# Optimization experiments

Measured on AMD Instinct MI355X. Metric: run time of the kernel, lower is better.

## Reference

```python
import jax, jax.numpy as jnp
import numpy as np

N_SRC = 50000
N_DST = 50000
D = 64
E = 800000


def setup_inputs() -> dict:
    key = jax.random.key(0)
    k1, k2, k3, k4, k5 = jax.random.split(key, 5)
    return {
        "h_src": jax.random.normal(k1, (N_SRC, D), dtype=jnp.float32),
        "h_dst": jax.random.normal(k2, (N_DST, D), dtype=jnp.float32),
        "src_idx": jax.random.randint(k3, (E,), 0, N_SRC, dtype=jnp.int64)
        if jax.config.read("jax_enable_x64")
        else jax.random.randint(k3, (E,), 0, N_SRC, dtype=jnp.int32),
        "dst_idx": jax.random.randint(k4, (E,), 0, N_DST, dtype=jnp.int32),
        "W_src": jax.random.normal(k5, (D, D), dtype=jnp.float32) * (2.0 / np.sqrt(2 * D)),  # xavier_normal w/ relu gain
        "b_src": jnp.zeros((D,), dtype=jnp.float32),
    }


def reference(h_src, h_dst, src_idx, dst_idx, W_src, b_src):
    # --- edge attention logits: u_mul_v (elementwise), shape [E, D] ---
    e = h_src[src_idx] * h_dst[dst_idx]
    # --- edge_softmax: softmax over incoming edges of each dst node, per feature dim ---
    emax = jax.ops.segment_max(e, dst_idx, num_segments=N_DST)  # [N_dst, D]
    emax = jnp.where(jnp.isfinite(emax), emax, 0.0)  # empty segments -> -inf; neutralize
    ex = jnp.exp(e - emax[dst_idx])  # [E, D]
    denom = jax.ops.segment_sum(ex, dst_idx, num_segments=N_DST)  # [N_dst, D]
    alpha = ex / denom[dst_idx]  # [E, D]
    # --- transformed src features: relu(W x + b), viewed as [N_src, H=1, D] ---
    feat_src = jax.nn.relu(h_src @ W_src.T + b_src)  # [N_src, D]
    # --- u_mul_e + sum aggregation (H=1 broadcast) ---
    m = feat_src[src_idx] * alpha  # [E, D]
    rst = jax.ops.segment_sum(m, dst_idx, num_segments=N_DST)  # [N_dst, D]
    return rst[:, None, :]  # [N_dst, num_heads=1, out_feats] (dropout in eval mode)
```

## Files before the change

### kernel.cpp

```cpp
#include <hip/hip_runtime.h>
#include <math.h>
#include <stdint.h>

#define D 64
#define WSZ 32
#define WSHIFT 5
#define QCAP 1024
#define EPT 16
#define NWMAX 2048

typedef __attribute__((ext_vector_type(8))) short bf16x8;
typedef __attribute__((ext_vector_type(4))) float f32x4;

__device__ inline ushort bf16_rne_u(float v) {
    uint32_t u = __float_as_uint(v);
    return (ushort)((u + 0x7FFFu + ((u >> 16) & 1u)) >> 16);
}

__global__ __launch_bounds__(256) void prep_kernel(const float* __restrict__ h,
                                                   const float* __restrict__ W,
                                                   const float* __restrict__ b,
                                                   const int* __restrict__ src_idx,
                                                   const int* __restrict__ dst_idx,
                                                   uint32_t* __restrict__ packed,
                                                   int* __restrict__ qcnt,
                                                   uint32_t* __restrict__ queue,
                                                   int Nsrc, int Ndst, int E, int packBlocks) {
    __shared__ ushort hT[64 * 64];
    __shared__ ushort wT[64 * 64];
    __shared__ float bs[64];
    __shared__ int wcount[NWMAX];
    __shared__ int wbase[NWMAX];

    if ((int)blockIdx.x < packBlocks) {
        const int t = threadIdx.x;
        const int R0 = blockIdx.x * 64;

        if (t < 64) bs[t] = b[t];
#pragma unroll
        for (int k = 0; k < 4; ++k) {
            int f4 = k * 256 + t;
            int row = f4 >> 4;
            int c4 = (f4 & 15) * 4;
            int grow = min(R0 + row, Nsrc - 1);
            float4 v = reinterpret_cast<const float4*>(h)[(size_t)grow * 16 + (f4 & 15)];
            hT[row * 64 + c4 + 0] = bf16_rne_u(v.x);
            hT[row * 64 + c4 + 1] = bf16_rne_u(v.y);
            hT[row * 64 + c4 + 2] = bf16_rne_u(v.z);
            hT[row * 64 + c4 + 3] = bf16_rne_u(v.w);
            float4 w = reinterpret_cast<const float4*>(W)[f4];
            wT[row * 64 + c4 + 0] = bf16_rne_u(w.x);
            wT[row * 64 + c4 + 1] = bf16_rne_u(w.y);
            wT[row * 64 + c4 + 2] = bf16_rne_u(w.z);
            wT[row * 64 + c4 + 3] = bf16_rne_u(w.w);
        }
        __syncthreads();

        const int wave = t >> 6;
        const int lane = t & 63;
        const int m = lane & 15;
        const int quad = lane >> 4;

        bf16x8 afrag[2];
#pragma unroll
        for (int ks = 0; ks < 2; ++ks)
            afrag[ks] = *reinterpret_cast<const bf16x8*>(&hT[(wave * 16 + m) * 64 + ks * 32 + quad * 8]);

#pragma unroll
        for (int nt = 0; nt < 4; ++nt) {
            const int c0 = nt * 16;
            f32x4 acc = {0.f, 0.f, 0.f, 0.f};
#pragma unroll
            for (int ks = 0; ks < 2; ++ks) {
                bf16x8 bfrag = *reinterpret_cast<const bf16x8*>(&wT[(c0 + m) * 64 + ks * 32 + quad * 8]);
                acc = __builtin_amdgcn_mfma_f32_16x16x32_bf16(afrag[ks], bfrag, acc, 0, 0, 0);
            }
            const int col = c0 + m;
            const float bias = bs[col];
#pragma unroll
            for (int reg = 0; reg < 4; ++reg) {
                const int tr = wave * 16 + quad * 4 + reg;
                const int row = R0 + tr;
                if (row < Nsrc) {
                    float f = fmaxf(acc[reg] + bias, 0.f);
                    uint32_t val = (uint32_t)hT[tr * 64 + col] | ((uint32_t)bf16_rne_u(f) << 16);
                    __builtin_nontemporal_store(val, &packed[(size_t)row * D + col]);
                }
            }
        }
    } else {
        const int bid = (int)blockIdx.x - packBlocks;
        const int t = threadIdx.x;
        for (int k = t; k < NWMAX; k += 256) wcount[k] = 0;
        __syncthreads();

        const int i = bid * 256 + t;
        const int e0 = i * EPT;
        const bool full = (e0 + EPT <= E);

        int4 d0, d1, d2, d3, s0, s1, s2, s3;
        if (full) {
            const int4* dp = reinterpret_cast<const int4*>(dst_idx) + i * 4;
            const int4* sp = reinterpret_cast<const int4*>(src_idx) + i * 4;
            d0 = dp[0]; d1 = dp[1]; d2 = dp[2]; d3 = dp[3];
            s0 = sp[0]; s1 = sp[1]; s2 = sp[2]; s3 = sp[3];
            atomicAdd(&wcount[d0.x >> WSHIFT], 1); atomicAdd(&wcount[d0.y >> WSHIFT], 1);
            atomicAdd(&wcount[d0.z >> WSHIFT], 1); atomicAdd(&wcount[d0.w >> WSHIFT], 1);
            atomicAdd(&wcount[d1.x >> WSHIFT], 1); atomicAdd(&wcount[d1.y >> WSHIFT], 1);
            atomicAdd(&wcount[d1.z >> WSHIFT], 1); atomicAdd(&wcount[d1.w >> WSHIFT], 1);
            atomicAdd(&wcount[d2.x >> WSHIFT], 1); atomicAdd(&wcount[d2.y >> WSHIFT], 1);
            atomicAdd(&wcount[d2.z >> WSHIFT], 1); atomicAdd(&wcount[d2.w >> WSHIFT], 1);
            atomicAdd(&wcount[d3.x >> WSHIFT], 1); atomicAdd(&wcount[d3.y >> WSHIFT], 1);
            atomicAdd(&wcount[d3.z >> WSHIFT], 1); atomicAdd(&wcount[d3.w >> WSHIFT], 1);
        } else {
            for (int e = e0; e < E; ++e) atomicAdd(&wcount[dst_idx[e] >> WSHIFT], 1);
        }
        __syncthreads();

        for (int k = t; k < NWMAX; k += 256) {
            int c = wcount[k];
            wbase[k] = (c > 0) ? atomicAdd(&qcnt[k], c) : 0;
        }
        __syncthreads();

#define EMIT(dv, sv)                                                            \
        {                                                                       \
            int w_ = (dv) >> WSHIFT;                                            \
            int pos_ = atomicAdd(&wbase[w_], 1);                                \
            if (pos_ < QCAP)                                                    \
                queue[(size_t)w_ * QCAP + pos_] =                               \
                    (uint32_t)(sv) | ((uint32_t)((dv) & (WSZ - 1)) << 16);      \
        }
        if (full) {
            EMIT(d0.x, s0.x) EMIT(d0.y, s0.y) EMIT(d0.z, s0.z) EMIT(d0.w, s0.w)
            EMIT(d1.x, s1.x) EMIT(d1.y, s1.y) EMIT(d1.z, s1.z) EMIT(d1.w, s1.w)
            EMIT(d2.x, s2.x) EMIT(d2.y, s2.y) EMIT(d2.z, s2.z) EMIT(d2.w, s2.w)
            EMIT(d3.x, s3.x) EMIT(d3.y, s3.y) EMIT(d3.z, s3.z) EMIT(d3.w, s3.w)
        } else {
            for (int e = e0; e < E; ++e) { EMIT(dst_idx[e], src_idx[e]) }
        }
#undef EMIT
    }
}

__device__ inline void stepd(uint32_t u, float y, float& l, float& a) {
    float x = __uint_as_float(u << 16);
    float f = __uint_as_float(u & 0xFFFF0000u);
    float pe = __expf(x * y);
    l += pe;
    a += pe * f;
}

__device__ inline void step4(uint4 u, const float4& y, float4& l, float4& a) {
    stepd(u.x, y.x, l.x, a.x);
    stepd(u.y, y.y, l.y, a.y);
    stepd(u.z, y.z, l.z, a.z);
    stepd(u.w, y.w, l.w, a.w);
}

__global__ __launch_bounds__(256) void sortmain_kernel(const uint32_t* __restrict__ queue,
                                                       const int* __restrict__ qcnt,
                                                       const uint32_t* __restrict__ packed,
                                                       const float* __restrict__ h_dst,
                                                       float* __restrict__ out, int Ndst) {
    __shared__ uint32_t ent[QCAP];
    __shared__ ushort srt[QCAP];
    __shared__ int hist[WSZ], sc[WSZ], cur[WSZ];
    const int w = blockIdx.x;
    const int t = threadIdx.x;
    const int n = min(qcnt[w], QCAP);

    for (int k = t; k < n; k += 256) ent[k] = queue[(size_t)w * QCAP + k];
    if (t < WSZ) hist[t] = 0;
    __syncthreads();
    for (int k = t; k < n; k += 256) atomicAdd(&hist[(ent[k] >> 16) & (WSZ - 1)], 1);
    __syncthreads();
    if (t < WSZ) sc[t] = hist[t];
    __syncthreads();
    for (int off = 1; off < WSZ; off <<= 1) {
        int v = (t >= off && t < WSZ) ? sc[t - off] : 0;
        __syncthreads();
        if (t < WSZ) sc[t] += v;
        __syncthreads();
    }
    if (t < WSZ) cur[t] = sc[t] - hist[t];
    __syncthreads();
    for (int k = t; k < n; k += 256) {
        uint32_t e = ent[k];
        int dl = (e >> 16) & (WSZ - 1);
        int pos = atomicAdd(&cur[dl], 1);
        srt[pos] = (ushort)(e & 0xFFFFu);
    }
    __syncthreads();

    const int g = t >> 4;
    const int q = t & 15;
#pragma unroll
    for (int rep = 0; rep < WSZ / 16; ++rep) {
        const int dl = rep * 16 + g;
        const int j = w * WSZ + dl;
        if (j >= Ndst) continue;

        const float4 y = reinterpret_cast<const float4*>(h_dst + (size_t)j * D)[q];
        const int cnt = hist[dl];
        const int base = sc[dl] - cnt;

        float4 l0 = make_float4(0.f, 0.f, 0.f, 0.f), a0 = l0;
        float4 l1 = l0, a1 = l0, l2 = l0, a2 = l0, l3 = l0, a3 = l0;

        int p = 0;
        for (; p + 3 < cnt; p += 4) {
            uint32_t s0 = srt[base + p], s1 = srt[base + p + 1];
            uint32_t s2 = srt[base + p + 2], s3 = srt[base + p + 3];
            uint4 u0 = reinterpret_cast<const uint4*>(packed + (size_t)s0 * D)[q];
            uint4 u1 = reinterpret_cast<const uint4*>(packed + (size_t)s1 * D)[q];
            uint4 u2 = reinterpret_cast<const uint4*>(packed + (size_t)s2 * D)[q];
            uint4 u3 = reinterpret_cast<const uint4*>(packed + (size_t)s3 * D)[q];
            step4(u0, y, l0, a0);
            step4(u1, y, l1, a1);
            step4(u2, y, l2, a2);
            step4(u3, y, l3, a3);
        }
        for (; p < cnt; ++p) {
            uint32_t s0 = srt[base + p];
            uint4 u0 = reinterpret_cast<const uint4*>(packed + (size_t)s0 * D)[q];
            step4(u0, y, l0, a0);
        }

        l0.x += l1.x + l2.x + l3.x; a0.x += a1.x + a2.x + a3.x;
        l0.y += l1.y + l2.y + l3.y; a0.y += a1.y + a2.y + a3.y;
        l0.z += l1.z + l2.z + l3.z; a0.z += a1.z + a2.z + a3.z;
        l0.w += l1.w + l2.w + l3.w; a0.w += a1.w + a2.w + a3.w;

        float4 o;
        o.x = (l0.x > 0.f) ? a0.x / l0.x : 0.f;
        o.y = (l0.y > 0.f) ? a0.y / l0.y : 0.f;
        o.z = (l0.z > 0.f) ? a0.z / l0.z : 0.f;
        o.w = (l0.w > 0.f) ? a0.w / l0.w : 0.f;
        reinterpret_cast<float4*>(out + (size_t)j * D)[q] = o;
    }
}

extern "C" void kernel_launch(void* const* d_in, const int* in_sizes, int n_in,
                              void* d_out, int out_size, void* d_ws, size_t ws_size,
                              hipStream_t stream) {
    const float* h_src = (const float*)d_in[0];
    const float* h_dst = (const float*)d_in[1];
    const int* src_idx = (const int*)d_in[2];
    const int* dst_idx = (const int*)d_in[3];
    const float* W_src = (const float*)d_in[4];
    const float* b_src = (const float*)d_in[5];
    float* out = (float*)d_out;

    const int Nsrc = in_sizes[0] / D;
    const int Ndst = in_sizes[1] / D;
    const int E = in_sizes[2];
    const int NW = (Ndst + WSZ - 1) >> WSHIFT;

    const int packBlocks = (Nsrc + 63) / 64;
    const int binBlocks = (E + 256 * EPT - 1) / (256 * EPT);

    uint32_t* packed   = (uint32_t*)d_ws;
    int*      qcnt     = (int*)(packed + (size_t)Nsrc * D);
    uint32_t* queue    = (uint32_t*)(qcnt + NWMAX);

    hipMemsetAsync(qcnt, 0, sizeof(int) * NWMAX, stream);

    prep_kernel<<<packBlocks + binBlocks, 256, 0, stream>>>(
        h_src, W_src, b_src, src_idx, dst_idx, packed, qcnt, queue,
        Nsrc, Ndst, E, packBlocks);
    sortmain_kernel<<<NW, 256, 0, stream>>>(queue, qcnt, packed, h_dst, out, Ndst);
}
```

Baseline: 127.1 us.

## Fuse prep and sort/aggregate kernels into one cooperative persistent kernel

Merges the pack/bin kernel and the per-window sort+aggregate kernel into a single persistent cooperative kernel. Blocks loop over tasks, then meet at a grid-wide sync instead of a kernel boundary, with shared memory unioned across phases. This removes one kernel launch and its drain and fill, at the cost of a grid barrier and a grid capped at the occupancy limit. It also drops the nontemporal store on packed so the data can stay in cache for the gather phase.

```diff
diff --git a/kernel.cpp b/kernel.cpp
--- a/kernel.cpp
+++ b/kernel.cpp
@@ -1,6 +1,9 @@
 #include <hip/hip_runtime.h>
+#include <hip/hip_cooperative_groups.h>
 #include <math.h>
 #include <stdint.h>
+
+namespace cg = cooperative_groups;
 
 #define D 64
 #define WSZ 32
@@ -17,132 +20,6 @@
     return (ushort)((u + 0x7FFFu + ((u >> 16) & 1u)) >> 16);
 }
 
-__global__ __launch_bounds__(256) void prep_kernel(const float* __restrict__ h,
-                                                   const float* __restrict__ W,
-                                                   const float* __restrict__ b,
-                                                   const int* __restrict__ src_idx,
-                                                   const int* __restrict__ dst_idx,
-                                                   uint32_t* __restrict__ packed,
-                                                   int* __restrict__ qcnt,
-                                                   uint32_t* __restrict__ queue,
-                                                   int Nsrc, int Ndst, int E, int packBlocks) {
-    __shared__ ushort hT[64 * 64];
-    __shared__ ushort wT[64 * 64];
-    __shared__ float bs[64];
-    __shared__ int wcount[NWMAX];
-    __shared__ int wbase[NWMAX];
-
-    if ((int)blockIdx.x < packBlocks) {
-        const int t = threadIdx.x;
-        const int R0 = blockIdx.x * 64;
-
-        if (t < 64) bs[t] = b[t];
-#pragma unroll
-        for (int k = 0; k < 4; ++k) {
-            int f4 = k * 256 + t;
-            int row = f4 >> 4;
-            int c4 = (f4 & 15) * 4;
-            int grow = min(R0 + row, Nsrc - 1);
-            float4 v = reinterpret_cast<const float4*>(h)[(size_t)grow * 16 + (f4 & 15)];
-            hT[row * 64 + c4 + 0] = bf16_rne_u(v.x);
-            hT[row * 64 + c4 + 1] = bf16_rne_u(v.y);
-            hT[row * 64 + c4 + 2] = bf16_rne_u(v.z);
-            hT[row * 64 + c4 + 3] = bf16_rne_u(v.w);
-            float4 w = reinterpret_cast<const float4*>(W)[f4];
-            wT[row * 64 + c4 + 0] = bf16_rne_u(w.x);
-            wT[row * 64 + c4 + 1] = bf16_rne_u(w.y);
-            wT[row * 64 + c4 + 2] = bf16_rne_u(w.z);
-            wT[row * 64 + c4 + 3] = bf16_rne_u(w.w);
-        }
-        __syncthreads();
-
-        const int wave = t >> 6;
-        const int lane = t & 63;
-        const int m = lane & 15;
-        const int quad = lane >> 4;
-
-        bf16x8 afrag[2];
-#pragma unroll
-        for (int ks = 0; ks < 2; ++ks)
-            afrag[ks] = *reinterpret_cast<const bf16x8*>(&hT[(wave * 16 + m) * 64 + ks * 32 + quad * 8]);
-
-#pragma unroll
-        for (int nt = 0; nt < 4; ++nt) {
-            const int c0 = nt * 16;
-            f32x4 acc = {0.f, 0.f, 0.f, 0.f};
-#pragma unroll
-            for (int ks = 0; ks < 2; ++ks) {
-                bf16x8 bfrag = *reinterpret_cast<const bf16x8*>(&wT[(c0 + m) * 64 + ks * 32 + quad * 8]);
-                acc = __builtin_amdgcn_mfma_f32_16x16x32_bf16(afrag[ks], bfrag, acc, 0, 0, 0);
-            }
-            const int col = c0 + m;
-            const float bias = bs[col];
-#pragma unroll
-            for (int reg = 0; reg < 4; ++reg) {
-                const int tr = wave * 16 + quad * 4 + reg;
-                const int row = R0 + tr;
-                if (row < Nsrc) {
-                    float f = fmaxf(acc[reg] + bias, 0.f);
-                    uint32_t val = (uint32_t)hT[tr * 64 + col] | ((uint32_t)bf16_rne_u(f) << 16);
-                    __builtin_nontemporal_store(val, &packed[(size_t)row * D + col]);
-                }
-            }
-        }
-    } else {
-        const int bid = (int)blockIdx.x - packBlocks;
-        const int t = threadIdx.x;
-        for (int k = t; k < NWMAX; k += 256) wcount[k] = 0;
-        __syncthreads();
-
-        const int i = bid * 256 + t;
-        const int e0 = i * EPT;
-        const bool full = (e0 + EPT <= E);
-
-        int4 d0, d1, d2, d3, s0, s1, s2, s3;
-        if (full) {
-            const int4* dp = reinterpret_cast<const int4*>(dst_idx) + i * 4;
-            const int4* sp = reinterpret_cast<const int4*>(src_idx) + i * 4;
-            d0 = dp[0]; d1 = dp[1]; d2 = dp[2]; d3 = dp[3];
-            s0 = sp[0]; s1 = sp[1]; s2 = sp[2]; s3 = sp[3];
-            atomicAdd(&wcount[d0.x >> WSHIFT], 1); atomicAdd(&wcount[d0.y >> WSHIFT], 1);
-            atomicAdd(&wcount[d0.z >> WSHIFT], 1); atomicAdd(&wcount[d0.w >> WSHIFT], 1);
-            atomicAdd(&wcount[d1.x >> WSHIFT], 1); atomicAdd(&wcount[d1.y >> WSHIFT], 1);
-            atomicAdd(&wcount[d1.z >> WSHIFT], 1); atomicAdd(&wcount[d1.w >> WSHIFT], 1);
-            atomicAdd(&wcount[d2.x >> WSHIFT], 1); atomicAdd(&wcount[d2.y >> WSHIFT], 1);
-            atomicAdd(&wcount[d2.z >> WSHIFT], 1); atomicAdd(&wcount[d2.w >> WSHIFT], 1);
-            atomicAdd(&wcount[d3.x >> WSHIFT], 1); atomicAdd(&wcount[d3.y >> WSHIFT], 1);
-            atomicAdd(&wcount[d3.z >> WSHIFT], 1); atomicAdd(&wcount[d3.w >> WSHIFT], 1);
-        } else {
-            for (int e = e0; e < E; ++e) atomicAdd(&wcount[dst_idx[e] >> WSHIFT], 1);
-        }
-        __syncthreads();
-
-        for (int k = t; k < NWMAX; k += 256) {
-            int c = wcount[k];
-            wbase[k] = (c > 0) ? atomicAdd(&qcnt[k], c) : 0;
-        }
-        __syncthreads();
-
-#define EMIT(dv, sv)                                                            \
-        {                                                                       \
-            int w_ = (dv) >> WSHIFT;                                            \
-            int pos_ = atomicAdd(&wbase[w_], 1);                                \
-            if (pos_ < QCAP)                                                    \
-                queue[(size_t)w_ * QCAP + pos_] =                               \
-                    (uint32_t)(sv) | ((uint32_t)((dv) & (WSZ - 1)) << 16);      \
-        }
-        if (full) {
-            EMIT(d0.x, s0.x) EMIT(d0.y, s0.y) EMIT(d0.z, s0.z) EMIT(d0.w, s0.w)
-            EMIT(d1.x, s1.x) EMIT(d1.y, s1.y) EMIT(d1.z, s1.z) EMIT(d1.w, s1.w)
-            EMIT(d2.x, s2.x) EMIT(d2.y, s2.y) EMIT(d2.z, s2.z) EMIT(d2.w, s2.w)
-            EMIT(d3.x, s3.x) EMIT(d3.y, s3.y) EMIT(d3.z, s3.z) EMIT(d3.w, s3.w)
-        } else {
-            for (int e = e0; e < E; ++e) { EMIT(dst_idx[e], src_idx[e]) }
-        }
-#undef EMIT
-    }
-}
-
 __device__ inline void stepd(uint32_t u, float y, float& l, float& a) {
     float x = __uint_as_float(u << 16);
     float f = __uint_as_float(u & 0xFFFF0000u);
@@ -158,86 +35,214 @@
     stepd(u.w, y.w, l.w, a.w);
 }
 
-__global__ __launch_bounds__(256) void sortmain_kernel(const uint32_t* __restrict__ queue,
-                                                       const int* __restrict__ qcnt,
-                                                       const uint32_t* __restrict__ packed,
-                                                       const float* __restrict__ h_dst,
-                                                       float* __restrict__ out, int Ndst) {
-    __shared__ uint32_t ent[QCAP];
-    __shared__ ushort srt[QCAP];
-    __shared__ int hist[WSZ], sc[WSZ], cur[WSZ];
-    const int w = blockIdx.x;
+__global__ __launch_bounds__(256, 4) void fused_kernel(
+        const float* __restrict__ h, const float* __restrict__ W,
+        const float* __restrict__ b,
+        const int* __restrict__ src_idx, const int* __restrict__ dst_idx,
+        const float* __restrict__ h_dst,
+        uint32_t* __restrict__ packed, int* __restrict__ qcnt,
+        uint32_t* __restrict__ queue, float* __restrict__ out,
+        int Nsrc, int Ndst, int E, int packBlocks, int binBlocks, int NW) {
+    __shared__ union {
+        struct { ushort hT[64 * 64]; ushort wT[64 * 64]; float bs[64]; } pk;
+        struct { int wcount[NWMAX]; int wbase[NWMAX]; } bn;
+        struct { uint32_t ent[QCAP]; ushort srt[QCAP];
+                 int hist[WSZ]; int sc[WSZ]; int cur[WSZ]; } sm;
+    } u;
+
     const int t = threadIdx.x;
-    const int n = min(qcnt[w], QCAP);
-
-    for (int k = t; k < n; k += 256) ent[k] = queue[(size_t)w * QCAP + k];
-    if (t < WSZ) hist[t] = 0;
-    __syncthreads();
-    for (int k = t; k < n; k += 256) atomicAdd(&hist[(ent[k] >> 16) & (WSZ - 1)], 1);
-    __syncthreads();
-    if (t < WSZ) sc[t] = hist[t];
-    __syncthreads();
-    for (int off = 1; off < WSZ; off <<= 1) {
-        int v = (t >= off && t < WSZ) ? sc[t - off] : 0;
-        __syncthreads();
-        if (t < WSZ) sc[t] += v;
-        __syncthreads();
+    const int tasks = packBlocks + binBlocks;
+
+    for (int task = blockIdx.x; task < tasks; task += gridDim.x) {
+        __syncthreads();
+        if (task < packBlocks) {
+            const int R0 = task * 64;
+            if (t < 64) u.pk.bs[t] = b[t];
+#pragma unroll
+            for (int k = 0; k < 4; ++k) {
+                int f4 = k * 256 + t;
+                int row = f4 >> 4;
+                int c4 = (f4 & 15) * 4;
+                int grow = min(R0 + row, Nsrc - 1);
+                float4 v = reinterpret_cast<const float4*>(h)[(size_t)grow * 16 + (f4 & 15)];
+                u.pk.hT[row * 64 + c4 + 0] = bf16_rne_u(v.x);
+                u.pk.hT[row * 64 + c4 + 1] = bf16_rne_u(v.y);
+                u.pk.hT[row * 64 + c4 + 2] = bf16_rne_u(v.z);
+                u.pk.hT[row * 64 + c4 + 3] = bf16_rne_u(v.w);
+                float4 w = reinterpret_cast<const float4*>(W)[f4];
+                u.pk.wT[row * 64 + c4 + 0] = bf16_rne_u(w.x);
+                u.pk.wT[row * 64 + c4 + 1] = bf16_rne_u(w.y);
+                u.pk.wT[row * 64 + c4 + 2] = bf16_rne_u(w.z);
+                u.pk.wT[row * 64 + c4 + 3] = bf16_rne_u(w.w);
+            }
+            __syncthreads();
+
+            const int wave = t >> 6;
+            const int lane = t & 63;
+            const int m = lane & 15;
+            const int quad = lane >> 4;
+
+            bf16x8 afrag[2];
+#pragma unroll
+            for (int ks = 0; ks < 2; ++ks)
+                afrag[ks] = *reinterpret_cast<const bf16x8*>(
+                    &u.pk.hT[(wave * 16 + m) * 64 + ks * 32 + quad * 8]);
+
+#pragma unroll
+            for (int nt = 0; nt < 4; ++nt) {
+                const int c0 = nt * 16;
+                f32x4 acc = {0.f, 0.f, 0.f, 0.f};
+#pragma unroll
+                for (int ks = 0; ks < 2; ++ks) {
+                    bf16x8 bfrag = *reinterpret_cast<const bf16x8*>(
+                        &u.pk.wT[(c0 + m) * 64 + ks * 32 + quad * 8]);
+                    acc = __builtin_amdgcn_mfma_f32_16x16x32_bf16(afrag[ks], bfrag, acc, 0, 0, 0);
+                }
+                const int col = c0 + m;
+                const float bias = u.pk.bs[col];
+#pragma unroll
+                for (int reg = 0; reg < 4; ++reg) {
+                    const int tr = wave * 16 + quad * 4 + reg;
+                    const int row = R0 + tr;
+                    if (row < Nsrc) {
+                        float f = fmaxf(acc[reg] + bias, 0.f);
+                        uint32_t val = (uint32_t)u.pk.hT[tr * 64 + col] |
+                                       ((uint32_t)bf16_rne_u(f) << 16);
+                        packed[(size_t)row * D + col] = val;
+                    }
+                }
+            }
+        } else {
+            const int bid = task - packBlocks;
+            for (int k = t; k < NWMAX; k += 256) u.bn.wcount[k] = 0;
+            __syncthreads();
+
+            const int i = bid * 256 + t;
+            const int e0 = i * EPT;
+            const bool full = (e0 + EPT <= E);
+
+            int4 d0, d1, d2, d3, s0, s1, s2, s3;
+            if (full) {
+                const int4* dp = reinterpret_cast<const int4*>(dst_idx) + i * 4;
+                const int4* sp = reinterpret_cast<const int4*>(src_idx) + i * 4;
+                d0 = dp[0]; d1 = dp[1]; d2 = dp[2]; d3 = dp[3];
+                s0 = sp[0]; s1 = sp[1]; s2 = sp[2]; s3 = sp[3];
+                atomicAdd(&u.bn.wcount[d0.x >> WSHIFT], 1); atomicAdd(&u.bn.wcount[d0.y >> WSHIFT], 1);
+                atomicAdd(&u.bn.wcount[d0.z >> WSHIFT], 1); atomicAdd(&u.bn.wcount[d0.w >> WSHIFT], 1);
+                atomicAdd(&u.bn.wcount[d1.x >> WSHIFT], 1); atomicAdd(&u.bn.wcount[d1.y >> WSHIFT], 1);
+                atomicAdd(&u.bn.wcount[d1.z >> WSHIFT], 1); atomicAdd(&u.bn.wcount[d1.w >> WSHIFT], 1);
+                atomicAdd(&u.bn.wcount[d2.x >> WSHIFT], 1); atomicAdd(&u.bn.wcount[d2.y >> WSHIFT], 1);
+                atomicAdd(&u.bn.wcount[d2.z >> WSHIFT], 1); atomicAdd(&u.bn.wcount[d2.w >> WSHIFT], 1);
+                atomicAdd(&u.bn.wcount[d3.x >> WSHIFT], 1); atomicAdd(&u.bn.wcount[d3.y >> WSHIFT], 1);
+                atomicAdd(&u.bn.wcount[d3.z >> WSHIFT], 1); atomicAdd(&u.bn.wcount[d3.w >> WSHIFT], 1);
+            } else {
+                for (int e = e0; e < E; ++e) atomicAdd(&u.bn.wcount[dst_idx[e] >> WSHIFT], 1);
+            }
+            __syncthreads();
+
+            for (int k = t; k < NWMAX; k += 256) {
+                int c = u.bn.wcount[k];
+                u.bn.wbase[k] = (c > 0) ? atomicAdd(&qcnt[k], c) : 0;
+            }
+            __syncthreads();
+
+#define EMIT(dv, sv)                                                            \
+            {                                                                   \
+                int w_ = (dv) >> WSHIFT;                                        \
+                int pos_ = atomicAdd(&u.bn.wbase[w_], 1);                       \
+                if (pos_ < QCAP)                                                \
+                    queue[(size_t)w_ * QCAP + pos_] =                           \
+                        (uint32_t)(sv) | ((uint32_t)((dv) & (WSZ - 1)) << 16);  \
+            }
+            if (full) {
+                EMIT(d0.x, s0.x) EMIT(d0.y, s0.y) EMIT(d0.z, s0.z) EMIT(d0.w, s0.w)
+                EMIT(d1.x, s1.x) EMIT(d1.y, s1.y) EMIT(d1.z, s1.z) EMIT(d1.w, s1.w)
+                EMIT(d2.x, s2.x) EMIT(d2.y, s2.y) EMIT(d2.z, s2.z) EMIT(d2.w, s2.w)
+                EMIT(d3.x, s3.x) EMIT(d3.y, s3.y) EMIT(d3.z, s3.z) EMIT(d3.w, s3.w)
+            } else {
+                for (int e = e0; e < E; ++e) { EMIT(dst_idx[e], src_idx[e]) }
+            }
+#undef EMIT
+        }
     }
-    if (t < WSZ) cur[t] = sc[t] - hist[t];
-    __syncthreads();
-    for (int k = t; k < n; k += 256) {
-        uint32_t e = ent[k];
-        int dl = (e >> 16) & (WSZ - 1);
-        int pos = atomicAdd(&cur[dl], 1);
-        srt[pos] = (ushort)(e & 0xFFFFu);
-    }
-    __syncthreads();
+
+    __threadfence();
+    cg::this_grid().sync();
 
     const int g = t >> 4;
     const int q = t & 15;
-#pragma unroll
-    for (int rep = 0; rep < WSZ / 16; ++rep) {
-        const int dl = rep * 16 + g;
-        const int j = w * WSZ + dl;
-        if (j >= Ndst) continue;
-
-        const float4 y = reinterpret_cast<const float4*>(h_dst + (size_t)j * D)[q];
-        const int cnt = hist[dl];
-        const int base = sc[dl] - cnt;
-
-        float4 l0 = make_float4(0.f, 0.f, 0.f, 0.f), a0 = l0;
-        float4 l1 = l0, a1 = l0, l2 = l0, a2 = l0, l3 = l0, a3 = l0;
-
-        int p = 0;
-        for (; p + 3 < cnt; p += 4) {
-            uint32_t s0 = srt[base + p], s1 = srt[base + p + 1];
-            uint32_t s2 = srt[base + p + 2], s3 = srt[base + p + 3];
-            uint4 u0 = reinterpret_cast<const uint4*>(packed + (size_t)s0 * D)[q];
-            uint4 u1 = reinterpret_cast<const uint4*>(packed + (size_t)s1 * D)[q];
-            uint4 u2 = reinterpret_cast<const uint4*>(packed + (size_t)s2 * D)[q];
-            uint4 u3 = reinterpret_cast<const uint4*>(packed + (size_t)s3 * D)[q];
-            step4(u0, y, l0, a0);
-            step4(u1, y, l1, a1);
-            step4(u2, y, l2, a2);
-            step4(u3, y, l3, a3);
-        }
-        for (; p < cnt; ++p) {
-            uint32_t s0 = srt[base + p];
-            uint4 u0 = reinterpret_cast<const uint4*>(packed + (size_t)s0 * D)[q];
-            step4(u0, y, l0, a0);
-        }
-
-        l0.x += l1.x + l2.x + l3.x; a0.x += a1.x + a2.x + a3.x;
-        l0.y += l1.y + l2.y + l3.y; a0.y += a1.y + a2.y + a3.y;
-        l0.z += l1.z + l2.z + l3.z; a0.z += a1.z + a2.z + a3.z;
-        l0.w += l1.w + l2.w + l3.w; a0.w += a1.w + a2.w + a3.w;
-
-        float4 o;
-        o.x = (l0.x > 0.f) ? a0.x / l0.x : 0.f;
-        o.y = (l0.y > 0.f) ? a0.y / l0.y : 0.f;
-        o.z = (l0.z > 0.f) ? a0.z / l0.z : 0.f;
-        o.w = (l0.w > 0.f) ? a0.w / l0.w : 0.f;
-        reinterpret_cast<float4*>(out + (size_t)j * D)[q] = o;
+
+    for (int w = blockIdx.x; w < NW; w += gridDim.x) {
+        __syncthreads();
+        const int n = min(qcnt[w], QCAP);
+
+        for (int k = t; k < n; k += 256) u.sm.ent[k] = queue[(size_t)w * QCAP + k];
+        if (t < WSZ) u.sm.hist[t] = 0;
+        __syncthreads();
+        for (int k = t; k < n; k += 256) atomicAdd(&u.sm.hist[(u.sm.ent[k] >> 16) & (WSZ - 1)], 1);
+        __syncthreads();
+        if (t < WSZ) u.sm.sc[t] = u.sm.hist[t];
+        __syncthreads();
+        for (int off = 1; off < WSZ; off <<= 1) {
+            int v = (t >= off && t < WSZ) ? u.sm.sc[t - off] : 0;
+            __syncthreads();
+            if (t < WSZ) u.sm.sc[t] += v;
+            __syncthreads();
+        }
+        if (t < WSZ) u.sm.cur[t] = u.sm.sc[t] - u.sm.hist[t];
+        __syncthreads();
+        for (int k = t; k < n; k += 256) {
+            uint32_t e = u.sm.ent[k];
+            int dl = (e >> 16) & (WSZ - 1);
+            int pos = atomicAdd(&u.sm.cur[dl], 1);
+            u.sm.srt[pos] = (ushort)(e & 0xFFFFu);
+        }
+        __syncthreads();
+
+#pragma unroll
+        for (int rep = 0; rep < WSZ / 16; ++rep) {
+            const int dl = rep * 16 + g;
+            const int j = w * WSZ + dl;
+            if (j >= Ndst) continue;
+
+            const float4 y = reinterpret_cast<const float4*>(h_dst + (size_t)j * D)[q];
+            const int cnt = u.sm.hist[dl];
+            const int base = u.sm.sc[dl] - cnt;
+
+            float4 l0 = make_float4(0.f, 0.f, 0.f, 0.f), a0 = l0;
+            float4 l1 = l0, a1 = l0, l2 = l0, a2 = l0, l3 = l0, a3 = l0;
+
+            int p = 0;
+            for (; p + 3 < cnt; p += 4) {
+                uint32_t s0 = u.sm.srt[base + p],     s1 = u.sm.srt[base + p + 1];
+                uint32_t s2 = u.sm.srt[base + p + 2], s3 = u.sm.srt[base + p + 3];
+                uint4 u0 = reinterpret_cast<const uint4*>(packed + (size_t)s0 * D)[q];
+                uint4 u1 = reinterpret_cast<const uint4*>(packed + (size_t)s1 * D)[q];
+                uint4 u2 = reinterpret_cast<const uint4*>(packed + (size_t)s2 * D)[q];
+                uint4 u3 = reinterpret_cast<const uint4*>(packed + (size_t)s3 * D)[q];
+                step4(u0, y, l0, a0);
+                step4(u1, y, l1, a1);
+                step4(u2, y, l2, a2);
+                step4(u3, y, l3, a3);
+            }
+            for (; p < cnt; ++p) {
+                uint32_t s0 = u.sm.srt[base + p];
+                uint4 u0 = reinterpret_cast<const uint4*>(packed + (size_t)s0 * D)[q];
+                step4(u0, y, l0, a0);
+            }
+
+            l0.x += l1.x + l2.x + l3.x; a0.x += a1.x + a2.x + a3.x;
+            l0.y += l1.y + l2.y + l3.y; a0.y += a1.y + a2.y + a3.y;
+            l0.z += l1.z + l2.z + l3.z; a0.z += a1.z + a2.z + a3.z;
+            l0.w += l1.w + l2.w + l3.w; a0.w += a1.w + a2.w + a3.w;
+
+            float4 o;
+            o.x = (l0.x > 0.f) ? a0.x / l0.x : 0.f;
+            o.y = (l0.y > 0.f) ? a0.y / l0.y : 0.f;
+            o.z = (l0.z > 0.f) ? a0.z / l0.z : 0.f;
+            o.w = (l0.w > 0.f) ? a0.w / l0.w : 0.f;
+            reinterpret_cast<float4*>(out + (size_t)j * D)[q] = o;
+        }
     }
 }
 
@@ -254,11 +259,11 @@
 
     const int Nsrc = in_sizes[0] / D;
     const int Ndst = in_sizes[1] / D;
-    const int E = in_sizes[2];
+    int E = in_sizes[2];
     const int NW = (Ndst + WSZ - 1) >> WSHIFT;
 
-    const int packBlocks = (Nsrc + 63) / 64;
-    const int binBlocks = (E + 256 * EPT - 1) / (256 * EPT);
+    int packBlocks = (Nsrc + 63) / 64;
+    int binBlocks = (E + 256 * EPT - 1) / (256 * EPT);
 
     uint32_t* packed   = (uint32_t*)d_ws;
     int*      qcnt     = (int*)(packed + (size_t)Nsrc * D);
@@ -266,8 +271,22 @@
 
     hipMemsetAsync(qcnt, 0, sizeof(int) * NWMAX, stream);
 
-    prep_kernel<<<packBlocks + binBlocks, 256, 0, stream>>>(
-        h_src, W_src, b_src, src_idx, dst_idx, packed, qcnt, queue,
-        Nsrc, Ndst, E, packBlocks);
-    sortmain_kernel<<<NW, 256, 0, stream>>>(queue, qcnt, packed, h_dst, out, Ndst);
-}
+    static int blocksPerCU = 0;
+    if (blocksPerCU == 0) {
+        hipOccupancyMaxActiveBlocksPerMultiprocessor(&blocksPerCU, fused_kernel, 256, 0);
+        if (blocksPerCU <= 0) blocksPerCU = 1;
+    }
+    const int tasks = packBlocks + binBlocks;
+    int want = tasks > NW ? tasks : NW;
+    int grid = blocksPerCU * 256;
+    if (grid > want) grid = want;
+
+    int Nsrc_ = Nsrc, Ndst_ = Ndst, E_ = E, pb_ = packBlocks, bb_ = binBlocks, NW_ = NW;
+    const float* h_ = h_src; const float* W_ = W_src; const float* b_ = b_src;
+    const int* si_ = src_idx; const int* di_ = dst_idx; const float* hd_ = h_dst;
+    uint32_t* pk_ = packed; int* qc_ = qcnt; uint32_t* qu_ = queue; float* out_ = out;
+    void* args[] = { &h_, &W_, &b_, &si_, &di_, &hd_, &pk_, &qc_, &qu_, &out_,
+                     &Nsrc_, &Ndst_, &E_, &pb_, &bb_, &NW_ };
+    hipLaunchCooperativeKernel((const void*)fused_kernel, dim3(grid), dim3(256),
+                               args, 0, stream);
+}
```

New measurement: 302.3 us. +137.8%, slower.
